# Kernel tuning notes

Measured on AMD Instinct MI355X. Metric: run time of the kernel, lower is better.

The kernel has to match this reference:

```python
import jax, jax.numpy as jnp
import numpy as np
import math

N_EMBD = 1024
D_STATE = 16
D_CONV = 4
EXPAND = 2
D_INNER = EXPAND * N_EMBD          # 2048
DT_RANK = math.ceil(N_EMBD / 16)   # 64
B, L = 2, 2048
LN_EPS = 1e-5


def setup_inputs() -> dict:
    key = jax.random.key(0)
    ks = jax.random.split(key, 12)
    s = lambda fan_in: 1.0 / np.sqrt(fan_in)
    x = jax.random.normal(ks[0], (B, L, N_EMBD), dtype=jnp.float32)
    ln_g = jnp.ones((N_EMBD,), jnp.float32)
    ln_b = jnp.zeros((N_EMBD,), jnp.float32)
    in_proj_w = jax.random.normal(ks[1], (2 * D_INNER, N_EMBD), jnp.float32) * s(N_EMBD)
    conv_w = jax.random.normal(ks[2], (D_INNER, 1, D_CONV), jnp.float32) * s(D_CONV)
    conv_b = jax.random.normal(ks[3], (D_INNER,), jnp.float32) * s(D_CONV)
    x_proj_w = jax.random.normal(ks[4], (DT_RANK + 2 * D_STATE, D_INNER), jnp.float32) * s(D_INNER)
    dt_proj_w = jax.random.normal(ks[5], (D_INNER, DT_RANK), jnp.float32) * s(DT_RANK)
    # dt bias initialized so softplus(dt) is in a reasonable range
    dt = jnp.exp(jax.random.uniform(ks[6], (D_INNER,)) * (np.log(0.1) - np.log(1e-3)) + np.log(1e-3))
    dt_proj_b = dt + jnp.log(-jnp.expm1(-dt))  # inverse softplus
    A_log = jnp.log(jnp.tile(jnp.arange(1, D_STATE + 1, dtype=jnp.float32)[None, :], (D_INNER, 1)))
    D = jnp.ones((D_INNER,), jnp.float32)
    out_proj_w = jax.random.normal(ks[7], (N_EMBD, D_INNER), jnp.float32) * s(D_INNER)
    return {"x": x, "ln_g": ln_g, "ln_b": ln_b, "in_proj_w": in_proj_w,
            "conv_w": conv_w, "conv_b": conv_b, "x_proj_w": x_proj_w,
            "dt_proj_w": dt_proj_w, "dt_proj_b": dt_proj_b,
            "A_log": A_log, "D": D, "out_proj_w": out_proj_w}


def _selective_scan(u, delta, A, Bt, Ct, D):
    # u, delta: (B, L, d_inner); A: (d_inner, d_state); Bt, Ct: (B, L, d_state)
    def step(h, inp):
        d_t, B_t, C_t, u_t = inp          # (B,di) (B,ds) (B,ds) (B,di)
        dA = jnp.exp(d_t[..., None] * A)                     # (B, di, ds)
        dBu = d_t[..., None] * B_t[:, None, :] * u_t[..., None]
        h = dA * h + dBu
        y = jnp.einsum('bds,bs->bd', h, C_t)
        return h, y
    h0 = jnp.zeros((u.shape[0], A.shape[0], A.shape[1]), u.dtype)
    xs = (jnp.swapaxes(delta, 0, 1), jnp.swapaxes(Bt, 0, 1),
          jnp.swapaxes(Ct, 0, 1), jnp.swapaxes(u, 0, 1))
    _, ys = jax.lax.scan(step, h0, xs)    # (L, B, di)
    return jnp.swapaxes(ys, 0, 1) + u * D


def reference(x, ln_g, ln_b, in_proj_w, conv_w, conv_b, x_proj_w,
              dt_proj_w, dt_proj_b, A_log, D, out_proj_w):
    # Pre-LayerNorm
    mu = jnp.mean(x, axis=-1, keepdims=True)
    var = jnp.var(x, axis=-1, keepdims=True)
    x_norm = (x - mu) * jax.lax.rsqrt(var + LN_EPS) * ln_g + ln_b

    # Input projection -> (u, res)
    xz = jnp.einsum('bld,ed->ble', x_norm, in_proj_w)        # (B, L, 2*di)
    u, res = jnp.split(xz, 2, axis=-1)

    # Causal depthwise conv1d over time
    u_c = jnp.swapaxes(u, 1, 2)                              # (B, di, L)
    u_c = jax.lax.conv_general_dilated(
        u_c, conv_w, window_strides=(1,), padding=[(D_CONV - 1, 0)],
        dimension_numbers=('NCH', 'OIH', 'NCH'), feature_group_count=D_INNER)
    u_c = jax.nn.silu(jnp.swapaxes(u_c, 1, 2) + conv_b)      # (B, L, di)

    # SSM parameterization
    x_dbl = jnp.einsum('bld,ed->ble', u_c, x_proj_w)         # (B, L, dt_rank + 2*ds)
    dt, Bt, Ct = jnp.split(x_dbl, [DT_RANK, DT_RANK + D_STATE], axis=-1)
    delta = jax.nn.softplus(jnp.einsum('blr,dr->bld', dt, dt_proj_w) + dt_proj_b)
    A = -jnp.exp(A_log)                                      # (di, ds)

    y = _selective_scan(u_c, delta, A, Bt, Ct, D)            # (B, L, di)
    y = y * jax.nn.silu(res)
    out = jnp.einsum('bld,ed->ble', y, out_proj_w)           # (B, L, n_embd)
    return x + out
```

## Files before the change

### kernel.cpp

```cpp
#include <hip/hip_runtime.h>
#include <hip/hip_bf16.h>
#include <math.h>

#define NE    1024
#define DI    2048
#define LSEQ  2048
#define NB    2
#define DS    16
#define DTR   64
#define XDW   96

#define CCH   64
#define TCH   (LSEQ/CCH)

#define SKX   8
#define XPROJ_PART (4096*96)

typedef __attribute__((ext_vector_type(8))) short short8;
typedef __attribute__((ext_vector_type(4))) float floatx4;

__device__ __forceinline__ float softplusf(float x) {
    return (x > 20.f) ? x : log1pf(expf(x));
}
__device__ __forceinline__ float softplus_fast(float x) {
    return (x > 20.f) ? x : __logf(1.f + __expf(x));
}
__device__ __forceinline__ float siluf(float x) {
    return x / (1.f + __expf(-x));
}

__device__ __forceinline__ void gld16(const void* g, void* l) {
    __builtin_amdgcn_global_load_lds(
        (const __attribute__((address_space(1))) unsigned int*)g,
        (__attribute__((address_space(3))) unsigned int*)l, 16, 0, 0);
}

#define F2BF_N1 (4096*1024/4)
#define F2BF_N2 (2048*1024/4)
#define F2BF_N3 (96*2048/4)
#define F2BF_N4 (2048*64/4)
#define LN_BLOCKS 4096
#define F2BF_BLOCKS ((F2BF_N1 + F2BF_N2 + F2BF_N3 + F2BF_N4) / 256)

__global__ __launch_bounds__(256) void prep_kernel(
    const float* __restrict__ x, const float* __restrict__ g,
    const float* __restrict__ b, __hip_bfloat16* __restrict__ xn,
    const float* __restrict__ s1, ushort4* __restrict__ d1,
    const float* __restrict__ s2, ushort4* __restrict__ d2,
    const float* __restrict__ s3, ushort4* __restrict__ d3,
    const float* __restrict__ s4, ushort4* __restrict__ d4)
{
    int tid = threadIdx.x;
    if (blockIdx.x >= LN_BLOCKS) {
        int i = (blockIdx.x - LN_BLOCKS) * 256 + tid;
        const float* src; ushort4* dst; int j;
        if (i < F2BF_N1)                           { src = s1; dst = d1; j = i; }
        else if (i < F2BF_N1 + F2BF_N2)            { src = s2; dst = d2; j = i - F2BF_N1; }
        else if (i < F2BF_N1 + F2BF_N2 + F2BF_N3)  { src = s3; dst = d3; j = i - F2BF_N1 - F2BF_N2; }
        else                                       { src = s4; dst = d4; j = i - F2BF_N1 - F2BF_N2 - F2BF_N3; }
        float4 v = ((const float4*)src)[j];
        union { __hip_bfloat16 h[4]; ushort4 u; } cv;
        cv.h[0] = __float2bfloat16(v.x);
        cv.h[1] = __float2bfloat16(v.y);
        cv.h[2] = __float2bfloat16(v.z);
        cv.h[3] = __float2bfloat16(v.w);
        dst[j] = cv.u;
        return;
    }
    int row = blockIdx.x;
    const float4* xr = (const float4*)(x + (size_t)row * NE);
    float4 v = xr[tid];
    float s  = v.x + v.y + v.z + v.w;
    float sq = v.x*v.x + v.y*v.y + v.z*v.z + v.w*v.w;
    #pragma unroll
    for (int off = 32; off > 0; off >>= 1) {
        s  += __shfl_down(s, off);
        sq += __shfl_down(sq, off);
    }
    __shared__ float ss[4], ssq[4];
    __shared__ float smu, srstd;
    int wv = tid >> 6, lane = tid & 63;
    if (lane == 0) { ss[wv] = s; ssq[wv] = sq; }
    __syncthreads();
    if (tid == 0) {
        float a = ss[0] + ss[1] + ss[2] + ss[3];
        float q = ssq[0] + ssq[1] + ssq[2] + ssq[3];
        float mu  = a * (1.f / NE);
        float var = q * (1.f / NE) - mu * mu;
        smu = mu; srstd = rsqrtf(var + 1e-5f);
    }
    __syncthreads();
    float mu = smu, rstd = srstd;
    float4 gv = ((const float4*)g)[tid];
    float4 bv = ((const float4*)b)[tid];
    union { __hip_bfloat16 h[4]; ushort4 u; } cv;
    cv.h[0] = __float2bfloat16((v.x - mu) * rstd * gv.x + bv.x);
    cv.h[1] = __float2bfloat16((v.y - mu) * rstd * gv.y + bv.y);
    cv.h[2] = __float2bfloat16((v.z - mu) * rstd * gv.z + bv.z);
    cv.h[3] = __float2bfloat16((v.w - mu) * rstd * gv.w + bv.w);
    ((ushort4*)xn)[row * 256 + tid] = cv.u;
}

template<bool BF16OUT>
__global__ __launch_bounds__(256) void gemm_bf16mm(
    const __hip_bfloat16* __restrict__ A,
    const __hip_bfloat16* __restrict__ W,
    void* __restrict__ Cv, int N, int K)
{
    __shared__ __hip_bfloat16 As[128 * 64];
    __shared__ __hip_bfloat16 Bs[128 * 64];
    int tid = threadIdx.x;
    int lane = tid & 63;
    int w = tid >> 6, wr = w >> 1, wc = w & 1;
    int row0 = blockIdx.y * 128, col0 = blockIdx.x * 128;

    int sr = tid >> 3, sc = tid & 7;
    int gc = sc ^ (sr & 7);
    const __hip_bfloat16* ag = A + (size_t)(row0 + sr) * K + gc * 8;
    const __hip_bfloat16* bg = W + (size_t)(col0 + sr) * K + gc * 8;
    char* la_st = (char*)As + w * 1024;
    char* lb_st = (char*)Bs + w * 1024;
    const size_t rs32 = (size_t)32 * K;

    floatx4 acc[4][4];
    #pragma unroll
    for (int i = 0; i < 4; ++i)
        #pragma unroll
        for (int j = 0; j < 4; ++j) acc[i][j] = (floatx4){0.f, 0.f, 0.f, 0.f};

    int m = lane & 15, kq = lane >> 4;
    int s0 = kq ^ (m & 7);
    int s1 = (4 + kq) ^ (m & 7);
    const char* la0 = (const char*)As + (wr * 64 + m) * 128 + s0 * 16;
    const char* la1 = (const char*)As + (wr * 64 + m) * 128 + s1 * 16;
    const char* lb0 = (const char*)Bs + (wc * 64 + m) * 128 + s0 * 16;
    const char* lb1 = (const char*)Bs + (wc * 64 + m) * 128 + s1 * 16;

    for (int k0 = 0; k0 < K; k0 += 64) {
        #pragma unroll
        for (int j = 0; j < 4; ++j) {
            gld16(ag + j * rs32, la_st + j * 4096);
            gld16(bg + j * rs32, lb_st + j * 4096);
        }
        ag += 64; bg += 64;
        __syncthreads();
        {
            short8 af[4], bf[4];
            #pragma unroll
            for (int i = 0; i < 4; ++i) {
                af[i] = *(const short8*)(la0 + i * 2048);
                bf[i] = *(const short8*)(lb0 + i * 2048);
            }
            #pragma unroll
            for (int i = 0; i < 4; ++i)
                #pragma unroll
                for (int j = 0; j < 4; ++j)
                    acc[i][j] = __builtin_amdgcn_mfma_f32_16x16x32_bf16(
                        af[i], bf[j], acc[i][j], 0, 0, 0);
        }
        {
            short8 af[4], bf[4];
            #pragma unroll
            for (int i = 0; i < 4; ++i) {
                af[i] = *(const short8*)(la1 + i * 2048);
                bf[i] = *(const short8*)(lb1 + i * 2048);
            }
            #pragma unroll
            for (int i = 0; i < 4; ++i)
                #pragma unroll
                for (int j = 0; j < 4; ++j)
                    acc[i][j] = __builtin_amdgcn_mfma_f32_16x16x32_bf16(
                        af[i], bf[j], acc[i][j], 0, 0, 0);
        }
        __syncthreads();
    }

    int crow = row0 + wr * 64 + kq * 4;
    int ccol = col0 + wc * 64 + m;
    #pragma unroll
    for (int i = 0; i < 4; ++i)
        #pragma unroll
        for (int j = 0; j < 4; ++j)
            #pragma unroll
            for (int r2 = 0; r2 < 4; ++r2) {
                size_t rr = (size_t)(crow + i * 16 + r2);
                int cc = ccol + j * 16;
                if (BF16OUT)
                    ((__hip_bfloat16*)Cv)[rr * N + cc] = __float2bfloat16(acc[i][j][r2]);
                else
                    ((float*)Cv)[rr * N + cc] = acc[i][j][r2];
            }
}

__global__ __launch_bounds__(256) void dtproj_mfma(
    const __hip_bfloat16* __restrict__ A,
    const __hip_bfloat16* __restrict__ W,
    const float* __restrict__ bias,
    __hip_bfloat16* __restrict__ dlt)
{
    __shared__ __hip_bfloat16 As[128 * 64];
    __shared__ __hip_bfloat16 Bs[128 * 64];
    int tid = threadIdx.x;
    int lane = tid & 63;
    int w = tid >> 6, wr = w >> 1, wc = w & 1;
    int row0 = blockIdx.y * 128, col0 = blockIdx.x * 128;
    const int K = DTR;

    int sr = tid >> 3, sc = tid & 7;
    int gc = sc ^ (sr & 7);
    const __hip_bfloat16* ag = A + (size_t)(row0 + sr) * K + gc * 8;
    const __hip_bfloat16* bg = W + (size_t)(col0 + sr) * K + gc * 8;
    char* la_st = (char*)As + w * 1024;
    char* lb_st = (char*)Bs + w * 1024;
    const size_t rs32 = (size_t)32 * K;

    #pragma unroll
    for (int j = 0; j < 4; ++j) {
        gld16(ag + j * rs32, la_st + j * 4096);
        gld16(bg + j * rs32, lb_st + j * 4096);
    }

    floatx4 acc[4][4];
    #pragma unroll
    for (int i = 0; i < 4; ++i)
        #pragma unroll
        for (int j = 0; j < 4; ++j) acc[i][j] = (floatx4){0.f, 0.f, 0.f, 0.f};

    int m = lane & 15, kq = lane >> 4;
    int s0 = kq ^ (m & 7);
    int s1 = (4 + kq) ^ (m & 7);
    const char* la0 = (const char*)As + (wr * 64 + m) * 128 + s0 * 16;
    const char* la1 = (const char*)As + (wr * 64 + m) * 128 + s1 * 16;
    const char* lb0 = (const char*)Bs + (wc * 64 + m) * 128 + s0 * 16;
    const char* lb1 = (const char*)Bs + (wc * 64 + m) * 128 + s1 * 16;
    __syncthreads();
    {
        short8 af[4], bf[4];
        #pragma unroll
        for (int i = 0; i < 4; ++i) {
            af[i] = *(const short8*)(la0 + i * 2048);
            bf[i] = *(const short8*)(lb0 + i * 2048);
        }
        #pragma unroll
        for (int i = 0; i < 4; ++i)
            #pragma unroll
            for (int j = 0; j < 4; ++j)
                acc[i][j] = __builtin_amdgcn_mfma_f32_16x16x32_bf16(
                    af[i], bf[j], acc[i][j], 0, 0, 0);
    }
    {
        short8 af[4], bf[4];
        #pragma unroll
        for (int i = 0; i < 4; ++i) {
            af[i] = *(const short8*)(la1 + i * 2048);
            bf[i] = *(const short8*)(lb1 + i * 2048);
        }
        #pragma unroll
        for (int i = 0; i < 4; ++i)
            #pragma unroll
            for (int j = 0; j < 4; ++j)
                acc[i][j] = __builtin_amdgcn_mfma_f32_16x16x32_bf16(
                    af[i], bf[j], acc[i][j], 0, 0, 0);
    }

    int crow = row0 + wr * 64 + kq * 4;
    int ccol = col0 + wc * 64 + m;
    float bj[4];
    #pragma unroll
    for (int j = 0; j < 4; ++j) bj[j] = bias[ccol + j * 16];
    #pragma unroll
    for (int i = 0; i < 4; ++i)
        #pragma unroll
        for (int j = 0; j < 4; ++j)
            #pragma unroll
            for (int r2 = 0; r2 < 4; ++r2) {
                size_t rr = (size_t)(crow + i * 16 + r2);
                int cc = ccol + j * 16;
                dlt[rr * DI + cc] =
                    __float2bfloat16(softplus_fast(acc[i][j][r2] + bj[j]));
            }
}

__global__ __launch_bounds__(256) void gemm_bf16_n128(
    const __hip_bfloat16* __restrict__ A,
    const __hip_bfloat16* __restrict__ W,
    const float* __restrict__ resid,
    float* __restrict__ C, int N, int K)
{
    __shared__ __hip_bfloat16 As[64 * 64];
    __shared__ __hip_bfloat16 Bs[128 * 64];
    int tid = threadIdx.x;
    int lane = tid & 63;
    int w = tid >> 6;
    int row0 = blockIdx.y * 64, col0 = blockIdx.x * 128;

    int sr = tid >> 3, sc = tid & 7;
    int gc = sc ^ (sr & 7);
    const __hip_bfloat16* ag = A + (size_t)(row0 + sr) * K + gc * 8;
    const __hip_bfloat16* bg = W + (size_t)(col0 + sr) * K + gc * 8;
    char* la_st = (char*)As + w * 1024;
    char* lb_st = (char*)Bs + w * 1024;
    const size_t rs32 = (size_t)32 * K;

    floatx4 acc[4][2];
    #pragma unroll
    for (int i = 0; i < 4; ++i)
        #pragma unroll
        for (int j = 0; j < 2; ++j) acc[i][j] = (floatx4){0.f, 0.f, 0.f, 0.f};

    int m = lane & 15, kq = lane >> 4;
    int s0 = kq ^ (m & 7);
    int s1 = (4 + kq) ^ (m & 7);
    const char* la0 = (const char*)As + m * 128 + s0 * 16;
    const char* la1 = (const char*)As + m * 128 + s1 * 16;
    const char* lb0 = (const char*)Bs + (w * 32 + m) * 128 + s0 * 16;
    const char* lb1 = (const char*)Bs + (w * 32 + m) * 128 + s1 * 16;

    for (int k0 = 0; k0 < K; k0 += 64) {
        gld16(ag,        la_st);
        gld16(ag + rs32, la_st + 4096);
        #pragma unroll
        for (int j = 0; j < 4; ++j)
            gld16(bg + j * rs32, lb_st + j * 4096);
        ag += 64; bg += 64;
        __syncthreads();
        {
            short8 af[4], bf[2];
            #pragma unroll
            for (int i = 0; i < 4; ++i) af[i] = *(const short8*)(la0 + i * 2048);
            #pragma unroll
            for (int j = 0; j < 2; ++j) bf[j] = *(const short8*)(lb0 + j * 2048);
            #pragma unroll
            for (int i = 0; i < 4; ++i)
                #pragma unroll
                for (int j = 0; j < 2; ++j)
                    acc[i][j] = __builtin_amdgcn_mfma_f32_16x16x32_bf16(
                        af[i], bf[j], acc[i][j], 0, 0, 0);
        }
        {
            short8 af[4], bf[2];
            #pragma unroll
            for (int i = 0; i < 4; ++i) af[i] = *(const short8*)(la1 + i * 2048);
            #pragma unroll
            for (int j = 0; j < 2; ++j) bf[j] = *(const short8*)(lb1 + j * 2048);
            #pragma unroll
            for (int i = 0; i < 4; ++i)
                #pragma unroll
                for (int j = 0; j < 2; ++j)
                    acc[i][j] = __builtin_amdgcn_mfma_f32_16x16x32_bf16(
                        af[i], bf[j], acc[i][j], 0, 0, 0);
        }
        __syncthreads();
    }

    int crow = row0 + kq * 4;
    int ccol = col0 + w * 32 + m;
    #pragma unroll
    for (int i = 0; i < 4; ++i)
        #pragma unroll
        for (int j = 0; j < 2; ++j)
            #pragma unroll
            for (int r2 = 0; r2 < 4; ++r2) {
                size_t rr = (size_t)(crow + i * 16 + r2);
                int cc = ccol + j * 16;
                C[rr * N + cc] = acc[i][j][r2] + resid[rr * N + cc];
            }
}

__global__ __launch_bounds__(256) void xproj_kernel(
    const __hip_bfloat16* __restrict__ A,
    const __hip_bfloat16* __restrict__ W,
    float* __restrict__ xpart)
{
    int tid = threadIdx.x;
    int lane = tid & 63;
    int w = tid >> 6;
    int kz = blockIdx.y;
    int row0 = blockIdx.x * 128 + w * 32;
    int m  = lane & 15;
    int kq = lane >> 4;

    floatx4 acc[2][6];
    #pragma unroll
    for (int i = 0; i < 2; ++i)
        #pragma unroll
        for (int j = 0; j < 6; ++j) acc[i][j] = (floatx4){0.f, 0.f, 0.f, 0.f};

    const __hip_bfloat16* a0 = A + (size_t)(row0 + m) * DI + kz * (DI / SKX) + kq * 8;
    const __hip_bfloat16* b0 = W + (size_t)m * DI + kz * (DI / SKX) + kq * 8;

    #pragma unroll
    for (int ks = 0; ks < (DI / SKX) / 32; ++ks) {
        short8 af0 = *(const short8*)(a0);
        short8 af1 = *(const short8*)(a0 + (size_t)16 * DI);
        #pragma unroll
        for (int j = 0; j < 6; ++j) {
            short8 bf = *(const short8*)(b0 + (size_t)j * 16 * DI);
            acc[0][j] = __builtin_amdgcn_mfma_f32_16x16x32_bf16(af0, bf, acc[0][j], 0, 0, 0);
            acc[1][j] = __builtin_amdgcn_mfma_f32_16x16x32_bf16(af1, bf, acc[1][j], 0, 0, 0);
        }
        a0 += 32; b0 += 32;
    }

    float* cp = xpart + (size_t)kz * XPROJ_PART;
    int crow = row0 + kq * 4;
    #pragma unroll
    for (int i = 0; i < 2; ++i)
        #pragma unroll
        for (int j = 0; j < 6; ++j)
            #pragma unroll
            for (int r = 0; r < 4; ++r)
                cp[(size_t)(crow + i * 16 + r) * XDW + j * 16 + m] = acc[i][j][r];
}

__global__ __launch_bounds__(256) void reduce8_kernel(
    const float* __restrict__ part, float* __restrict__ xdbl,
    __hip_bfloat16* __restrict__ dtx)
{
    int i = blockIdx.x * 256 + threadIdx.x;
    float s = 0.f;
    #pragma unroll
    for (int k = 0; k < SKX; ++k) s += part[(size_t)k * XPROJ_PART + i];
    xdbl[i] = s;
    int row = i / XDW;
    int col = i - row * XDW;
    if (col < DTR)
        dtx[(size_t)row * DTR + col] = __float2bfloat16(s);
}

__global__ __launch_bounds__(256) void conv_silu_kernel(
    const __hip_bfloat16* __restrict__ xz, const float* __restrict__ cw,
    const float* __restrict__ cb, ushort4* __restrict__ uc_bf)
{
    int i4 = blockIdx.x * 256 + threadIdx.x;
    int d4 = i4 & 511;
    int bt = i4 >> 9;
    int t  = bt & (LSEQ - 1);
    int d  = d4 * 4;
    float4 w0 = *(const float4*)(cw + (size_t)(d+0) * 4);
    float4 w1 = *(const float4*)(cw + (size_t)(d+1) * 4);
    float4 w2 = *(const float4*)(cw + (size_t)(d+2) * 4);
    float4 w3 = *(const float4*)(cw + (size_t)(d+3) * 4);
    const float* wt0 = (const float*)&w0;
    const float* wt1 = (const float*)&w1;
    const float* wt2 = (const float*)&w2;
    const float* wt3 = (const float*)&w3;
    float4 acc = *(const float4*)(cb + d);
    const __hip_bfloat16* base = xz + ((size_t)bt << 12) + d;
    #pragma unroll
    for (int k = 0; k < 4; ++k) {
        int tp = t - 3 + k;
        if (tp >= 0) {
            union { ushort4 u; __hip_bfloat16 h[4]; } raw;
            raw.u = *(const ushort4*)(base - ((size_t)(3 - k) << 12));
            acc.x = fmaf(wt0[k], __bfloat162float(raw.h[0]), acc.x);
            acc.y = fmaf(wt1[k], __bfloat162float(raw.h[1]), acc.y);
            acc.z = fmaf(wt2[k], __bfloat162float(raw.h[2]), acc.z);
            acc.w = fmaf(wt3[k], __bfloat162float(raw.h[3]), acc.w);
        }
    }
    union { __hip_bfloat16 h[4]; ushort4 u; } cv;
    cv.h[0] = __float2bfloat16(siluf(acc.x));
    cv.h[1] = __float2bfloat16(siluf(acc.y));
    cv.h[2] = __float2bfloat16(siluf(acc.z));
    cv.h[3] = __float2bfloat16(siluf(acc.w));
    uc_bf[i4] = cv.u;
}

template<bool FINAL>
__global__ __launch_bounds__(256) void scan_chunk_kernel(
    const __hip_bfloat16* __restrict__ dlt, const __hip_bfloat16* __restrict__ uc,
    const float* __restrict__ xdbl, const float* __restrict__ A_log,
    const float* __restrict__ Dp, const __hip_bfloat16* __restrict__ xz,
    float* __restrict__ P, float* __restrict__ S,
    __hip_bfloat16* __restrict__ y)
{
    __shared__ float sBC[TCH][32];
    int tid = threadIdx.x;
    int d = blockIdx.x * 256 + tid;
    int c = blockIdx.y;
    int b = blockIdx.z;
    int row0 = b * LSEQ + c * TCH;

    {
        int tt = tid >> 3, j4 = (tid & 7) * 4;
        const float4* src = (const float4*)(xdbl + (size_t)(row0 + tt) * XDW + DTR + j4);
        *(float4*)(&sBC[tt][j4]) = *src;
    }
    __syncthreads();

    float Ac[DS], h[DS], p[DS];
    #pragma unroll
    for (int s = 0; s < DS; ++s) {
        Ac[s] = -expf(A_log[(size_t)d * DS + s]);
        p[s] = 1.f;
    }
    size_t soff = (((size_t)b * CCH + c) * DI + d) * DS;
    if (FINAL) {
        #pragma unroll
        for (int s = 0; s < DS; ++s) h[s] = S[soff + s];
    } else {
        #pragma unroll
        for (int s = 0; s < DS; ++s) h[s] = 0.f;
    }
    float Dd = Dp[d];
    size_t ix = (size_t)row0 * DI + d;
    for (int tt = 0; tt < TCH; ++tt) {
        float dv = __bfloat162float(dlt[ix]);
        float ut = __bfloat162float(uc[ix]);
        float du = dv * ut;
        float yacc = 0.f;
        #pragma unroll
        for (int s = 0; s < DS; ++s) {
            float e = __expf(dv * Ac[s]);
            h[s] = fmaf(e, h[s], du * sBC[tt][s]);
            if (FINAL) yacc = fmaf(h[s], sBC[tt][16 + s], yacc);
            else       p[s] *= e;
        }
        if (FINAL) {
            float res = __bfloat162float(xz[((size_t)(row0 + tt) << 12) + DI + d]);
            y[ix] = __float2bfloat16(fmaf(ut, Dd, yacc) * siluf(res));
        }
        ix += DI;
    }
    if (!FINAL) {
        #pragma unroll
        for (int s = 0; s < DS; ++s) { P[soff + s] = p[s]; S[soff + s] = h[s]; }
    }
}

__global__ __launch_bounds__(256) void scan_combine_kernel(
    const float* __restrict__ P, float* __restrict__ S)
{
    int idx = blockIdx.x * 256 + threadIdx.x;
    int b = idx >> 15;
    int rest = idx & 32767;
    float h = 0.f;
    for (int c = 0; c < CCH; ++c) {
        size_t off = (((size_t)b * CCH + c) << 15) + rest;
        float tmp = S[off];
        float pv  = P[off];
        S[off] = h;
        h = fmaf(pv, h, tmp);
    }
}

extern "C" void kernel_launch(void* const* d_in, const int* in_sizes, int n_in,
                              void* d_out, int out_size, void* d_ws, size_t ws_size,
                              hipStream_t stream)
{
    const float* x        = (const float*)d_in[0];
    const float* ln_g     = (const float*)d_in[1];
    const float* ln_b     = (const float*)d_in[2];
    const float* in_w     = (const float*)d_in[3];
    const float* conv_w   = (const float*)d_in[4];
    const float* conv_b   = (const float*)d_in[5];
    const float* xproj_w  = (const float*)d_in[6];
    const float* dtproj_w = (const float*)d_in[7];
    const float* dtproj_b = (const float*)d_in[8];
    const float* A_log    = (const float*)d_in[9];
    const float* Dvec     = (const float*)d_in[10];
    const float* out_w    = (const float*)d_in[11];
    float* out = (float*)d_out;

    char* base = (char*)d_ws;
    __hip_bfloat16* xz_bf    = (__hip_bfloat16*)(base + 0);
    __hip_bfloat16* dlt_bf   = (__hip_bfloat16*)(base + 33554432);
    __hip_bfloat16* uc_bf    = (__hip_bfloat16*)(base + 67108864);
    float*          xdbl     = (float*)         (base + 83886080);
    float*          xpart    = (float*)         (base + 85458944);
    float*          Pch      = (float*)         (base + 85458944);
    float*          Sch      = (float*)         (base + 102236160);
    __hip_bfloat16* xnorm_bf = (__hip_bfloat16*)(base + 119013376);
    __hip_bfloat16* yb_bf    = (__hip_bfloat16*)(base + 127401984);
    __hip_bfloat16* inw_bf   = (__hip_bfloat16*)(base + 144179200);
    __hip_bfloat16* outw_bf  = (__hip_bfloat16*)(base + 152567808);
    __hip_bfloat16* xpw_bf   = (__hip_bfloat16*)(base + 156762112);
    __hip_bfloat16* dtx_bf   = (__hip_bfloat16*)(base + 157155328);
    __hip_bfloat16* dtw_bf   = (__hip_bfloat16*)(base + 157679616);

    const int R = NB * LSEQ;

    prep_kernel<<<LN_BLOCKS + F2BF_BLOCKS, 256, 0, stream>>>(
        x, ln_g, ln_b, xnorm_bf,
        in_w, (ushort4*)inw_bf, out_w, (ushort4*)outw_bf,
        xproj_w, (ushort4*)xpw_bf, dtproj_w, (ushort4*)dtw_bf);
    gemm_bf16mm<true><<<dim3((2*DI)/128, R/128), 256, 0, stream>>>(
        xnorm_bf, inw_bf, (void*)xz_bf, 2*DI, NE);
    conv_silu_kernel<<<(R * DI / 4) / 256, 256, 0, stream>>>(
        xz_bf, conv_w, conv_b, (ushort4*)uc_bf);
    xproj_kernel<<<dim3(R/128, SKX), 256, 0, stream>>>(uc_bf, xpw_bf, xpart);
    reduce8_kernel<<<(R * XDW) / 256, 256, 0, stream>>>(xpart, xdbl, dtx_bf);
    dtproj_mfma<<<dim3(DI/128, R/128), 256, 0, stream>>>(
        dtx_bf, dtw_bf, dtproj_b, dlt_bf);
    dim3 gScan(DI / 256, CCH, NB);
    scan_chunk_kernel<false><<<gScan, 256, 0, stream>>>(
        dlt_bf, uc_bf, xdbl, A_log, Dvec, xz_bf, Pch, Sch, yb_bf);
    scan_combine_kernel<<<(NB * DI * DS) / 256, 256, 0, stream>>>(Pch, Sch);
    scan_chunk_kernel<true><<<gScan, 256, 0, stream>>>(
        dlt_bf, uc_bf, xdbl, A_log, Dvec, xz_bf, Pch, Sch, yb_bf);
    gemm_bf16_n128<<<dim3(NE/128, R/64), 256, 0, stream>>>(
        yb_bf, outw_bf, x, out, NE, DI);
}
```

Measured before the change: 330.3 us.

## Widen in-proj GEMM tile to 128x256 and halve scan chunk count

The input-projection GEMM now uses a 128x256 output tile, so each wave holds a 64x128 accumulator, A fragments are reused across twice as many columns, and fewer blocks are launched. Launch bounds request two blocks per CU despite the larger register footprint. The scan chunk count drops from 64 to 32, so each chunk is 64 timesteps long. The B/C staging loop is updated to load twice as many rows per block, and the combine step has fewer chunk states to process. In exchange, the scan has less parallelism and longer serial loops, and the GEMM has fewer blocks in flight and higher register pressure.

```diff
diff --git a/kernel.cpp b/kernel.cpp
--- a/kernel.cpp
+++ b/kernel.cpp
@@ -10,7 +10,7 @@
 #define DTR   64
 #define XDW   96
 
-#define CCH   64
+#define CCH   32
 #define TCH   (LSEQ/CCH)
 
 #define SKX   8
@@ -19,9 +19,6 @@
 typedef __attribute__((ext_vector_type(8))) short short8;
 typedef __attribute__((ext_vector_type(4))) float floatx4;
 
-__device__ __forceinline__ float softplusf(float x) {
-    return (x > 20.f) ? x : log1pf(expf(x));
-}
 __device__ __forceinline__ float softplus_fast(float x) {
     return (x > 20.f) ? x : __logf(1.f + __expf(x));
 }
@@ -101,18 +98,17 @@
     ((ushort4*)xn)[row * 256 + tid] = cv.u;
 }
 
-template<bool BF16OUT>
-__global__ __launch_bounds__(256) void gemm_bf16mm(
+__global__ __launch_bounds__(256, 2) void gemm_bf16_in(
     const __hip_bfloat16* __restrict__ A,
     const __hip_bfloat16* __restrict__ W,
-    void* __restrict__ Cv, int N, int K)
+    __hip_bfloat16* __restrict__ C, int N, int K)
 {
     __shared__ __hip_bfloat16 As[128 * 64];
-    __shared__ __hip_bfloat16 Bs[128 * 64];
+    __shared__ __hip_bfloat16 Bs[256 * 64];
     int tid = threadIdx.x;
     int lane = tid & 63;
     int w = tid >> 6, wr = w >> 1, wc = w & 1;
-    int row0 = blockIdx.y * 128, col0 = blockIdx.x * 128;
+    int row0 = blockIdx.y * 128, col0 = blockIdx.x * 256;
 
     int sr = tid >> 3, sc = tid & 7;
     int gc = sc ^ (sr & 7);
@@ -122,53 +118,52 @@
     char* lb_st = (char*)Bs + w * 1024;
     const size_t rs32 = (size_t)32 * K;
 
-    floatx4 acc[4][4];
+    floatx4 acc[4][8];
     #pragma unroll
     for (int i = 0; i < 4; ++i)
         #pragma unroll
-        for (int j = 0; j < 4; ++j) acc[i][j] = (floatx4){0.f, 0.f, 0.f, 0.f};
+        for (int j = 0; j < 8; ++j) acc[i][j] = (floatx4){0.f, 0.f, 0.f, 0.f};
 
     int m = lane & 15, kq = lane >> 4;
     int s0 = kq ^ (m & 7);
     int s1 = (4 + kq) ^ (m & 7);
     const char* la0 = (const char*)As + (wr * 64 + m) * 128 + s0 * 16;
     const char* la1 = (const char*)As + (wr * 64 + m) * 128 + s1 * 16;
-    const char* lb0 = (const char*)Bs + (wc * 64 + m) * 128 + s0 * 16;
-    const char* lb1 = (const char*)Bs + (wc * 64 + m) * 128 + s1 * 16;
+    const char* lb0 = (const char*)Bs + (wc * 128 + m) * 128 + s0 * 16;
+    const char* lb1 = (const char*)Bs + (wc * 128 + m) * 128 + s1 * 16;
 
     for (int k0 = 0; k0 < K; k0 += 64) {
         #pragma unroll
-        for (int j = 0; j < 4; ++j) {
+        for (int j = 0; j < 4; ++j)
             gld16(ag + j * rs32, la_st + j * 4096);
+        #pragma unroll
+        for (int j = 0; j < 8; ++j)
             gld16(bg + j * rs32, lb_st + j * 4096);
-        }
         ag += 64; bg += 64;
         __syncthreads();
         {
-            short8 af[4], bf[4];
-            #pragma unroll
-            for (int i = 0; i < 4; ++i) {
-                af[i] = *(const short8*)(la0 + i * 2048);
-                bf[i] = *(const short8*)(lb0 + i * 2048);
-            }
+            short8 af[4], bf[8];
+            #pragma unroll
+            for (int i = 0; i < 4; ++i) af[i] = *(const short8*)(la0 + i * 2048);
+            #pragma unroll
+            for (int j = 0; j < 8; ++j) bf[j] = *(const short8*)(lb0 + j * 2048);
             #pragma unroll
             for (int i = 0; i < 4; ++i)
                 #pragma unroll
-                for (int j = 0; j < 4; ++j)
+                for (int j = 0; j < 8; ++j)
                     acc[i][j] = __builtin_amdgcn_mfma_f32_16x16x32_bf16(
                         af[i], bf[j], acc[i][j], 0, 0, 0);
         }
         {
-            short8 af[4], bf[4];
-            #pragma unroll
-            for (int i = 0; i < 4; ++i) {
-                af[i] = *(const short8*)(la1 + i * 2048);
-                bf[i] = *(const short8*)(lb1 + i * 2048);
-            }
+            short8 af[4], bf[8];
+            #pragma unroll
+            for (int i = 0; i < 4; ++i) af[i] = *(const short8*)(la1 + i * 2048);
+            #pragma unroll
+            for (int j = 0; j < 8; ++j) bf[j] = *(const short8*)(lb1 + j * 2048);
             #pragma unroll
             for (int i = 0; i < 4; ++i)
                 #pragma unroll
-                for (int j = 0; j < 4; ++j)
+                for (int j = 0; j < 8; ++j)
                     acc[i][j] = __builtin_amdgcn_mfma_f32_16x16x32_bf16(
                         af[i], bf[j], acc[i][j], 0, 0, 0);
         }
@@ -176,19 +171,16 @@
     }
 
     int crow = row0 + wr * 64 + kq * 4;
-    int ccol = col0 + wc * 64 + m;
+    int ccol = col0 + wc * 128 + m;
     #pragma unroll
     for (int i = 0; i < 4; ++i)
         #pragma unroll
-        for (int j = 0; j < 4; ++j)
+        for (int j = 0; j < 8; ++j)
             #pragma unroll
             for (int r2 = 0; r2 < 4; ++r2) {
                 size_t rr = (size_t)(crow + i * 16 + r2);
                 int cc = ccol + j * 16;
-                if (BF16OUT)
-                    ((__hip_bfloat16*)Cv)[rr * N + cc] = __float2bfloat16(acc[i][j][r2]);
-                else
-                    ((float*)Cv)[rr * N + cc] = acc[i][j][r2];
+                C[rr * N + cc] = __float2bfloat16(acc[i][j][r2]);
             }
 }
 
@@ -483,9 +475,13 @@
     int row0 = b * LSEQ + c * TCH;
 
     {
-        int tt = tid >> 3, j4 = (tid & 7) * 4;
-        const float4* src = (const float4*)(xdbl + (size_t)(row0 + tt) * XDW + DTR + j4);
-        *(float4*)(&sBC[tt][j4]) = *src;
+        #pragma unroll
+        for (int it = 0; it < 2; ++it) {
+            int li = it * 256 + tid;
+            int tt = li >> 3, j4 = (li & 7) * 4;
+            const float4* src = (const float4*)(xdbl + (size_t)(row0 + tt) * XDW + DTR + j4);
+            *(float4*)(&sBC[tt][j4]) = *src;
+        }
     }
     __syncthreads();
 
@@ -585,8 +581,8 @@
         x, ln_g, ln_b, xnorm_bf,
         in_w, (ushort4*)inw_bf, out_w, (ushort4*)outw_bf,
         xproj_w, (ushort4*)xpw_bf, dtproj_w, (ushort4*)dtw_bf);
-    gemm_bf16mm<true><<<dim3((2*DI)/128, R/128), 256, 0, stream>>>(
-        xnorm_bf, inw_bf, (void*)xz_bf, 2*DI, NE);
+    gemm_bf16_in<<<dim3((2*DI)/256, R/128), 256, 0, stream>>>(
+        xnorm_bf, inw_bf, xz_bf, 2*DI, NE);
     conv_silu_kernel<<<(R * DI / 4) / 256, 256, 0, stream>>>(
         xz_bf, conv_w, conv_b, (ushort4*)uc_bf);
     xproj_kernel<<<dim3(R/128, SKX), 256, 0, stream>>>(uc_bf, xpw_bf, xpart);
```

After: 322.4 us. 1.02x faster.
